# Performance work log

Hardware: AMD Instinct MI355X
Metric: run time of the kernel (lower is better)

The kernel has to match this reference:

```python
import jax, jax.numpy as jnp
import numpy as np

HIDDEN = 128

def setup_inputs() -> dict:
    key = jax.random.key(0)
    ks = jax.random.split(key, 7)
    B, T, I, O = 256, 512, 256, 1000
    s_ih = 1.0 / np.sqrt(HIDDEN)
    x = jax.random.normal(ks[0], (B, T, I), dtype=jnp.float32)
    W_ih = jax.random.uniform(ks[1], (HIDDEN, I), minval=-s_ih, maxval=s_ih, dtype=jnp.float32)
    W_hh = jax.random.uniform(ks[2], (HIDDEN, HIDDEN), minval=-s_ih, maxval=s_ih, dtype=jnp.float32)
    b_ih = jax.random.uniform(ks[3], (HIDDEN,), minval=-s_ih, maxval=s_ih, dtype=jnp.float32)
    b_hh = jax.random.uniform(ks[4], (HIDDEN,), minval=-s_ih, maxval=s_ih, dtype=jnp.float32)
    s_fc = 1.0 / np.sqrt(HIDDEN)
    W_fc = jax.random.uniform(ks[5], (O, HIDDEN), minval=-s_fc, maxval=s_fc, dtype=jnp.float32)
    b_fc = jax.random.uniform(ks[6], (O,), minval=-s_fc, maxval=s_fc, dtype=jnp.float32)
    return {"x": x, "W_ih": W_ih, "W_hh": W_hh, "b_ih": b_ih, "b_hh": b_hh, "W_fc": W_fc, "b_fc": b_fc}


def reference(x, W_ih, W_hh, b_ih, b_hh, W_fc, b_fc):
    B = x.shape[0]
    # Precompute input projection for all timesteps in one big GEMM: [B,T,H]
    xp = jnp.einsum('bti,hi->bth', x, W_ih) + b_ih + b_hh
    h0 = jnp.zeros((B, HIDDEN), dtype=x.dtype)

    def step(h, xp_t):
        h = jnp.tanh(xp_t + h @ W_hh.T)
        return h, None

    # scan over time axis; only the final hidden state feeds the fc head
    h_last, _ = jax.lax.scan(step, h0, jnp.swapaxes(xp, 0, 1))
    return h_last @ W_fc.T + b_fc
```

## Files before the change

### kernel.cpp

```cpp
#include <hip/hip_runtime.h>


#define HID    128
#define TSTEPS 512
#define BATCH  256
#define INDIM  256
#define ODIM   1000

typedef __attribute__((ext_vector_type(8))) short bf16x8;
typedef __attribute__((ext_vector_type(4))) float f32x4;

__device__ __forceinline__ unsigned fb(float f) { return __float_as_uint(f); }
__device__ __forceinline__ float    bf(unsigned u) { return __uint_as_float(u); }
__device__ __forceinline__ unsigned hipair(unsigned e0, unsigned e1) {
    return __builtin_amdgcn_perm(e1, e0, 0x07060302u);
}
__device__ __forceinline__ unsigned rne(unsigned u) {
    return u + 0x7FFFu + ((u >> 16) & 1u);
}
__device__ __forceinline__ float tanh_fast(float p) {
    float v = fminf(fmaxf(p, -15.f), 15.f);
    float e = __expf(2.f * v);
    return 1.f - 2.f * __builtin_amdgcn_rcpf(e + 1.f);
}

__global__ __launch_bounds__(256) void k_phase1(const float* __restrict__ x,
                                                const float* __restrict__ Wih,
                                                const float* __restrict__ bih,
                                                const float* __restrict__ bhh,
                                                float* __restrict__ xp) {
    __shared__ __align__(16) unsigned short xs[2][4096];
    __shared__ __align__(16) unsigned short whs[2][4096];
    __shared__ __align__(16) unsigned short wls[2][4096];

    const int tid  = threadIdx.x;
    const int wave = tid >> 6, lane = tid & 63;
    const int quad = lane >> 4, l16 = lane & 15;
    const int wm = wave >> 1, wn = wave & 1;
    const int m0 = blockIdx.x * 128;

    int srow[4], scol[4], sdst[4];
#pragma unroll
    for (int q = 0; q < 4; q++) {
        int li = q * 256 + tid;
        srow[q] = li >> 3;
        scol[q] = li & 7;
        sdst[q] = srow[q] * 32 + ((((scol[q] >> 1) ^ srow[q]) & 3) << 3) + ((scol[q] & 1) << 2);
    }

    float bias_v[4];
#pragma unroll
    for (int nt = 0; nt < 4; nt++) {
        int j = wn * 64 + nt * 16 + l16;
        bias_v[nt] = bih[j] + bhh[j];
    }

    float4 rx[4], rw[4];
#define LOAD_STAGE(KC)                                                              \
    {                                                                               \
        _Pragma("unroll") for (int q = 0; q < 4; q++) {                             \
            rx[q] = *(const float4*)(x + (size_t)(m0 + srow[q]) * INDIM + (KC) * 32 + scol[q] * 4); \
            rw[q] = *(const float4*)(Wih + (size_t)srow[q] * INDIM + (KC) * 32 + scol[q] * 4);      \
        }                                                                           \
    }
#define WRITE_STAGE(BUF)                                                            \
    {                                                                               \
        _Pragma("unroll") for (int q = 0; q < 4; q++) {                             \
            uint2 px;                                                               \
            px.x = hipair(rne(fb(rx[q].x)), rne(fb(rx[q].y)));                      \
            px.y = hipair(rne(fb(rx[q].z)), rne(fb(rx[q].w)));                      \
            *(uint2*)&xs[BUF][sdst[q]] = px;                                        \
            unsigned u0 = fb(rw[q].x) & 0xFFFF0000u, u1 = fb(rw[q].y) & 0xFFFF0000u;\
            unsigned u2 = fb(rw[q].z) & 0xFFFF0000u, u3 = fb(rw[q].w) & 0xFFFF0000u;\
            unsigned v0 = fb(rw[q].x - bf(u0)), v1 = fb(rw[q].y - bf(u1));          \
            unsigned v2 = fb(rw[q].z - bf(u2)), v3 = fb(rw[q].w - bf(u3));          \
            uint2 ph, pl;                                                           \
            ph.x = hipair(u0, u1); ph.y = hipair(u2, u3);                           \
            pl.x = hipair(v0, v1); pl.y = hipair(v2, v3);                           \
            *(uint2*)&whs[BUF][sdst[q]] = ph;                                       \
            *(uint2*)&wls[BUF][sdst[q]] = pl;                                       \
        }                                                                           \
    }

    f32x4 acc[4][4];
#pragma unroll
    for (int mt = 0; mt < 4; mt++)
#pragma unroll
        for (int nt = 0; nt < 4; nt++) {
            acc[mt][nt].x = 0.f; acc[mt][nt].y = 0.f;
            acc[mt][nt].z = 0.f; acc[mt][nt].w = 0.f;
        }

    LOAD_STAGE(0);
    WRITE_STAGE(0);
    __syncthreads();

    for (int kc = 0; kc < 8; kc++) {
        const int b = kc & 1;
        if (kc < 7) LOAD_STAGE(kc + 1);

        bf16x8 a[4], bh[4], bl[4];
#pragma unroll
        for (int mt = 0; mt < 4; mt++) {
            int row = wm * 64 + mt * 16 + l16;
            a[mt] = *(const bf16x8*)&xs[b][row * 32 + (((quad ^ row) & 3) << 3)];
        }
#pragma unroll
        for (int nt = 0; nt < 4; nt++) {
            int row = wn * 64 + nt * 16 + l16;
            int ad  = row * 32 + (((quad ^ row) & 3) << 3);
            bh[nt] = *(const bf16x8*)&whs[b][ad];
            bl[nt] = *(const bf16x8*)&wls[b][ad];
        }
#pragma unroll
        for (int mt = 0; mt < 4; mt++)
#pragma unroll
            for (int nt = 0; nt < 4; nt++) {
                acc[mt][nt] = __builtin_amdgcn_mfma_f32_16x16x32_bf16(a[mt], bh[nt], acc[mt][nt], 0, 0, 0);
                acc[mt][nt] = __builtin_amdgcn_mfma_f32_16x16x32_bf16(a[mt], bl[nt], acc[mt][nt], 0, 0, 0);
            }

        if (kc < 7) WRITE_STAGE(b ^ 1);
        __syncthreads();
    }

#pragma unroll
    for (int mt = 0; mt < 4; mt++)
#pragma unroll
        for (int nt = 0; nt < 4; nt++)
#pragma unroll
            for (int reg = 0; reg < 4; reg++) {
                int row = m0 + wm * 64 + mt * 16 + quad * 4 + reg;
                xp[(size_t)row * HID + wn * 64 + nt * 16 + l16] = acc[mt][nt][reg] + bias_v[nt];
            }
#undef LOAD_STAGE
#undef WRITE_STAGE
}

#define RNN_STEP3(TV, XQI, XQC, PB) {                                             \
    _Pragma("unroll") for (int reg = 0; reg < 4; reg++) {                         \
        float hv = tanh_fast(C[reg]);                                             \
        unsigned u = rne(fb(hv));                                                 \
        int m = quad * 4 + reg;                                                   \
        hp[PB][m * 128 + ((((jbase >> 3) ^ m) & 15) << 3) + (jbase & 7)] =        \
            (unsigned short)(u >> 16);                                            \
    }                                                                             \
    if ((TV) + 4 < TSTEPS) {                                                      \
        _Pragma("unroll") for (int reg = 0; reg < 4; reg++)                       \
            XQI[reg] = xpb[ib[reg] + ((TV) + 4) * HID];                           \
    }                                                                             \
    __syncthreads();                                                              \
    bf16x8 A[4];                                                                  \
    _Pragma("unroll") for (int kc = 0; kc < 4; kc++)                              \
        A[kc] = *(const bf16x8*)&hp[PB][l16 * 128 + ((((kc * 4 + quad) ^ l16) & 15) << 3)]; \
    f32x4 ch, cl;                                                                 \
    ch.x = XQC[0]; ch.y = XQC[1]; ch.z = XQC[2]; ch.w = XQC[3];                   \
    cl.x = 0.f; cl.y = 0.f; cl.z = 0.f; cl.w = 0.f;                               \
    _Pragma("unroll") for (int kc = 0; kc < 4; kc++) {                            \
        ch = __builtin_amdgcn_mfma_f32_16x16x32_bf16(A[kc], Bh[kc], ch, 0, 0, 0); \
        cl = __builtin_amdgcn_mfma_f32_16x16x32_bf16(A[kc], Bl[kc], cl, 0, 0, 0); \
    }                                                                             \
    C = ch + cl;                                                                  \
}

__global__ __launch_bounds__(512) void k_rnn3(const float* __restrict__ Whh,
                                              float* __restrict__ ws) {
    __shared__ __align__(16) unsigned short hp[2][16 * 128];
    const int tid  = threadIdx.x;
    const int wave = tid >> 6, lane = tid & 63;
    const int quad = lane >> 4, l16 = lane & 15;
    const int r0    = blockIdx.x * 16;
    const int jbase = wave * 16 + l16;

    bf16x8 Bh[4], Bl[4];
#pragma unroll
    for (int kc = 0; kc < 4; kc++) {
        const float* p = Whh + (size_t)jbase * HID + kc * 32 + quad * 8;
        float e[8];
        *(float4*)&e[0] = *(const float4*)p;
        *(float4*)&e[4] = *(const float4*)(p + 4);
        unsigned hu[8], lu[8];
#pragma unroll
        for (int i = 0; i < 8; i++) {
            unsigned u = fb(e[i]), hm = u & 0xFFFF0000u;
            hu[i] = hm;
            lu[i] = fb(e[i] - bf(hm));
        }
        union { unsigned u[4]; bf16x8 v; } th, tl;
#pragma unroll
        for (int q = 0; q < 4; q++) {
            th.u[q] = hipair(hu[2 * q], hu[2 * q + 1]);
            tl.u[q] = hipair(lu[2 * q], lu[2 * q + 1]);
        }
        Bh[kc] = th.v; Bl[kc] = tl.v;
    }

    const float* xpb = ws;
    int ib[4];
#pragma unroll
    for (int reg = 0; reg < 4; reg++)
        ib[reg] = (r0 + quad * 4 + reg) * (TSTEPS * HID) + jbase;

    f32x4 C;
    float xq0[4], xq1[4], xq2[4], xq3[4];
    C.x = xpb[ib[0]]; C.y = xpb[ib[1]]; C.z = xpb[ib[2]]; C.w = xpb[ib[3]];
#pragma unroll
    for (int reg = 0; reg < 4; reg++) {
        xq1[reg] = xpb[ib[reg] + 1 * HID];
        xq2[reg] = xpb[ib[reg] + 2 * HID];
        xq3[reg] = xpb[ib[reg] + 3 * HID];
    }

    for (int t = 0; t < 508; t += 4) {
        RNN_STEP3(t,     xq0, xq1, 0);
        RNN_STEP3(t + 1, xq1, xq2, 1);
        RNN_STEP3(t + 2, xq2, xq3, 0);
        RNN_STEP3(t + 3, xq3, xq0, 1);
    }
    RNN_STEP3(508, xq0, xq1, 0);
    RNN_STEP3(509, xq1, xq2, 1);
    RNN_STEP3(510, xq2, xq3, 0);

#pragma unroll
    for (int reg = 0; reg < 4; reg++)
        ws[ib[reg]] = tanh_fast(C[reg]);
}

__global__ __launch_bounds__(256) void k_fc(const float* __restrict__ ws,
                                            const float* __restrict__ Wfc,
                                            const float* __restrict__ bfc,
                                            float* __restrict__ out) {
    __shared__ float hb[HID];
    const int b   = blockIdx.x;
    const int tid = threadIdx.x;
    if (tid < HID) hb[tid] = ws[(size_t)b * (TSTEPS * HID) + tid];
    __syncthreads();

    for (int o = tid; o < ODIM; o += 256) {
        const float* wr = Wfc + (size_t)o * HID;
        float acc = 0.f;
#pragma unroll
        for (int q = 0; q < 32; q++) {
            float4 wv = *(const float4*)(wr + q * 4);
            float4 hv = *(const float4*)&hb[q * 4];
            acc += wv.x * hv.x + wv.y * hv.y + wv.z * hv.z + wv.w * hv.w;
        }
        out[(size_t)b * ODIM + o] = acc + bfc[o];
    }
}

extern "C" void kernel_launch(void* const* d_in, const int* in_sizes, int n_in,
                              void* d_out, int out_size, void* d_ws, size_t ws_size,
                              hipStream_t stream) {
    const float* x   = (const float*)d_in[0];
    const float* Wih = (const float*)d_in[1];
    const float* Whh = (const float*)d_in[2];
    const float* bih = (const float*)d_in[3];
    const float* bhh = (const float*)d_in[4];
    const float* Wfc = (const float*)d_in[5];
    const float* bfc = (const float*)d_in[6];
    float* out = (float*)d_out;
    float* ws  = (float*)d_ws;

    k_phase1<<<dim3(1024), dim3(256), 0, stream>>>(x, Wih, bih, bhh, ws);
    k_rnn3  <<<dim3(16),   dim3(512), 0, stream>>>(Whh, ws);
    k_fc    <<<dim3(BATCH), dim3(256), 0, stream>>>(ws, Wfc, bfc, out);
}
```

Baseline: 424.3 us.

## Switch GEMM and recurrence MFMAs from split bf16 to single fp16

Replaces the bf16 hi/lo weight split (two MFMAs per tile) with a single fp16 operand in both the input-projection GEMM and the recurrent step, halving MFMA count and LDS traffic for weights. The recurrence step now runs four MFMAs in two independent accumulator chains instead of eight. tanh clamping is removed and conversion uses packed round-toward-zero fp16. This risks accuracy drift from fp16 range and precision in the weights, activations and the 512-step recurrence.

```diff
diff --git a/kernel.cpp b/kernel.cpp
--- a/kernel.cpp
+++ b/kernel.cpp
@@ -7,21 +7,19 @@
 #define INDIM  256
 #define ODIM   1000
 
-typedef __attribute__((ext_vector_type(8))) short bf16x8;
-typedef __attribute__((ext_vector_type(4))) float f32x4;
-
-__device__ __forceinline__ unsigned fb(float f) { return __float_as_uint(f); }
-__device__ __forceinline__ float    bf(unsigned u) { return __uint_as_float(u); }
-__device__ __forceinline__ unsigned hipair(unsigned e0, unsigned e1) {
-    return __builtin_amdgcn_perm(e1, e0, 0x07060302u);
-}
-__device__ __forceinline__ unsigned rne(unsigned u) {
-    return u + 0x7FFFu + ((u >> 16) & 1u);
-}
-__device__ __forceinline__ float tanh_fast(float p) {
-    float v = fminf(fmaxf(p, -15.f), 15.f);
+typedef _Float16 f16x8 __attribute__((ext_vector_type(8)));
+typedef __fp16   fp16x2 __attribute__((ext_vector_type(2)));
+typedef float    f32x4 __attribute__((ext_vector_type(4)));
+
+__device__ __forceinline__ unsigned pk16(float a, float b) {
+    union { fp16x2 h; unsigned u; } t;
+    t.h = __builtin_amdgcn_cvt_pkrtz(a, b);
+    return t.u;
+}
+__device__ __forceinline__ float tanh_fast(float v) {
     float e = __expf(2.f * v);
-    return 1.f - 2.f * __builtin_amdgcn_rcpf(e + 1.f);
+    float r = __builtin_amdgcn_rcpf(e + 1.f);
+    return __builtin_fmaf(-2.f, r, 1.f);
 }
 
 __global__ __launch_bounds__(256) void k_phase1(const float* __restrict__ x,
@@ -29,9 +27,8 @@
                                                 const float* __restrict__ bih,
                                                 const float* __restrict__ bhh,
                                                 float* __restrict__ xp) {
-    __shared__ __align__(16) unsigned short xs[2][4096];
-    __shared__ __align__(16) unsigned short whs[2][4096];
-    __shared__ __align__(16) unsigned short wls[2][4096];
+    __shared__ __align__(16) _Float16 xs[2][4096];
+    __shared__ __align__(16) _Float16 wsm[2][4096];
 
     const int tid  = threadIdx.x;
     const int wave = tid >> 6, lane = tid & 63;
@@ -66,19 +63,11 @@
 #define WRITE_STAGE(BUF)                                                            \
     {                                                                               \
         _Pragma("unroll") for (int q = 0; q < 4; q++) {                             \
-            uint2 px;                                                               \
-            px.x = hipair(rne(fb(rx[q].x)), rne(fb(rx[q].y)));                      \
-            px.y = hipair(rne(fb(rx[q].z)), rne(fb(rx[q].w)));                      \
-            *(uint2*)&xs[BUF][sdst[q]] = px;                                        \
-            unsigned u0 = fb(rw[q].x) & 0xFFFF0000u, u1 = fb(rw[q].y) & 0xFFFF0000u;\
-            unsigned u2 = fb(rw[q].z) & 0xFFFF0000u, u3 = fb(rw[q].w) & 0xFFFF0000u;\
-            unsigned v0 = fb(rw[q].x - bf(u0)), v1 = fb(rw[q].y - bf(u1));          \
-            unsigned v2 = fb(rw[q].z - bf(u2)), v3 = fb(rw[q].w - bf(u3));          \
-            uint2 ph, pl;                                                           \
-            ph.x = hipair(u0, u1); ph.y = hipair(u2, u3);                           \
-            pl.x = hipair(v0, v1); pl.y = hipair(v2, v3);                           \
-            *(uint2*)&whs[BUF][sdst[q]] = ph;                                       \
-            *(uint2*)&wls[BUF][sdst[q]] = pl;                                       \
+            uint2 px, pw;                                                           \
+            px.x = pk16(rx[q].x, rx[q].y); px.y = pk16(rx[q].z, rx[q].w);           \
+            pw.x = pk16(rw[q].x, rw[q].y); pw.y = pk16(rw[q].z, rw[q].w);           \
+            *(uint2*)&xs[BUF][sdst[q]]  = px;                                       \
+            *(uint2*)&wsm[BUF][sdst[q]] = pw;                                       \
         }                                                                           \
     }
 
@@ -99,26 +88,22 @@
         const int b = kc & 1;
         if (kc < 7) LOAD_STAGE(kc + 1);
 
-        bf16x8 a[4], bh[4], bl[4];
+        f16x8 a[4], bw[4];
 #pragma unroll
         for (int mt = 0; mt < 4; mt++) {
             int row = wm * 64 + mt * 16 + l16;
-            a[mt] = *(const bf16x8*)&xs[b][row * 32 + (((quad ^ row) & 3) << 3)];
+            a[mt] = *(const f16x8*)&xs[b][row * 32 + (((quad ^ row) & 3) << 3)];
         }
 #pragma unroll
         for (int nt = 0; nt < 4; nt++) {
             int row = wn * 64 + nt * 16 + l16;
-            int ad  = row * 32 + (((quad ^ row) & 3) << 3);
-            bh[nt] = *(const bf16x8*)&whs[b][ad];
-            bl[nt] = *(const bf16x8*)&wls[b][ad];
+            bw[nt] = *(const f16x8*)&wsm[b][row * 32 + (((quad ^ row) & 3) << 3)];
         }
 #pragma unroll
         for (int mt = 0; mt < 4; mt++)
 #pragma unroll
-            for (int nt = 0; nt < 4; nt++) {
-                acc[mt][nt] = __builtin_amdgcn_mfma_f32_16x16x32_bf16(a[mt], bh[nt], acc[mt][nt], 0, 0, 0);
-                acc[mt][nt] = __builtin_amdgcn_mfma_f32_16x16x32_bf16(a[mt], bl[nt], acc[mt][nt], 0, 0, 0);
-            }
+            for (int nt = 0; nt < 4; nt++)
+                acc[mt][nt] = __builtin_amdgcn_mfma_f32_16x16x32_f16(a[mt], bw[nt], acc[mt][nt], 0, 0, 0);
 
         if (kc < 7) WRITE_STAGE(b ^ 1);
         __syncthreads();
@@ -137,62 +122,49 @@
 #undef WRITE_STAGE
 }
 
-#define RNN_STEP3(TV, XQI, XQC, PB) {                                             \
+#define RNN_STEP4(TV, XQI, XQC, PB) {                                             \
     _Pragma("unroll") for (int reg = 0; reg < 4; reg++) {                         \
         float hv = tanh_fast(C[reg]);                                             \
-        unsigned u = rne(fb(hv));                                                 \
         int m = quad * 4 + reg;                                                   \
         hp[PB][m * 128 + ((((jbase >> 3) ^ m) & 15) << 3) + (jbase & 7)] =        \
-            (unsigned short)(u >> 16);                                            \
+            (_Float16)hv;                                                         \
     }                                                                             \
     if ((TV) + 4 < TSTEPS) {                                                      \
         _Pragma("unroll") for (int reg = 0; reg < 4; reg++)                       \
             XQI[reg] = xpb[ib[reg] + ((TV) + 4) * HID];                           \
     }                                                                             \
     __syncthreads();                                                              \
-    bf16x8 A[4];                                                                  \
+    f16x8 A[4];                                                                   \
     _Pragma("unroll") for (int kc = 0; kc < 4; kc++)                              \
-        A[kc] = *(const bf16x8*)&hp[PB][l16 * 128 + ((((kc * 4 + quad) ^ l16) & 15) << 3)]; \
+        A[kc] = *(const f16x8*)&hp[PB][l16 * 128 + ((((kc * 4 + quad) ^ l16) & 15) << 3)]; \
     f32x4 ch, cl;                                                                 \
     ch.x = XQC[0]; ch.y = XQC[1]; ch.z = XQC[2]; ch.w = XQC[3];                   \
     cl.x = 0.f; cl.y = 0.f; cl.z = 0.f; cl.w = 0.f;                               \
-    _Pragma("unroll") for (int kc = 0; kc < 4; kc++) {                            \
-        ch = __builtin_amdgcn_mfma_f32_16x16x32_bf16(A[kc], Bh[kc], ch, 0, 0, 0); \
-        cl = __builtin_amdgcn_mfma_f32_16x16x32_bf16(A[kc], Bl[kc], cl, 0, 0, 0); \
-    }                                                                             \
+    ch = __builtin_amdgcn_mfma_f32_16x16x32_f16(A[0], Bf[0], ch, 0, 0, 0);        \
+    cl = __builtin_amdgcn_mfma_f32_16x16x32_f16(A[2], Bf[2], cl, 0, 0, 0);        \
+    ch = __builtin_amdgcn_mfma_f32_16x16x32_f16(A[1], Bf[1], ch, 0, 0, 0);        \
+    cl = __builtin_amdgcn_mfma_f32_16x16x32_f16(A[3], Bf[3], cl, 0, 0, 0);        \
     C = ch + cl;                                                                  \
 }
 
-__global__ __launch_bounds__(512) void k_rnn3(const float* __restrict__ Whh,
+__global__ __launch_bounds__(512) void k_rnn4(const float* __restrict__ Whh,
                                               float* __restrict__ ws) {
-    __shared__ __align__(16) unsigned short hp[2][16 * 128];
+    __shared__ __align__(16) _Float16 hp[2][16 * 128];
     const int tid  = threadIdx.x;
     const int wave = tid >> 6, lane = tid & 63;
     const int quad = lane >> 4, l16 = lane & 15;
     const int r0    = blockIdx.x * 16;
     const int jbase = wave * 16 + l16;
 
-    bf16x8 Bh[4], Bl[4];
+    f16x8 Bf[4];
 #pragma unroll
     for (int kc = 0; kc < 4; kc++) {
         const float* p = Whh + (size_t)jbase * HID + kc * 32 + quad * 8;
-        float e[8];
-        *(float4*)&e[0] = *(const float4*)p;
-        *(float4*)&e[4] = *(const float4*)(p + 4);
-        unsigned hu[8], lu[8];
-#pragma unroll
-        for (int i = 0; i < 8; i++) {
-            unsigned u = fb(e[i]), hm = u & 0xFFFF0000u;
-            hu[i] = hm;
-            lu[i] = fb(e[i] - bf(hm));
-        }
-        union { unsigned u[4]; bf16x8 v; } th, tl;
-#pragma unroll
-        for (int q = 0; q < 4; q++) {
-            th.u[q] = hipair(hu[2 * q], hu[2 * q + 1]);
-            tl.u[q] = hipair(lu[2 * q], lu[2 * q + 1]);
-        }
-        Bh[kc] = th.v; Bl[kc] = tl.v;
+        float4 e0 = *(const float4*)p, e1 = *(const float4*)(p + 4);
+        union { unsigned u[4]; f16x8 v; } t;
+        t.u[0] = pk16(e0.x, e0.y); t.u[1] = pk16(e0.z, e0.w);
+        t.u[2] = pk16(e1.x, e1.y); t.u[3] = pk16(e1.z, e1.w);
+        Bf[kc] = t.v;
     }
 
     const float* xpb = ws;
@@ -212,14 +184,14 @@
     }
 
     for (int t = 0; t < 508; t += 4) {
-        RNN_STEP3(t,     xq0, xq1, 0);
-        RNN_STEP3(t + 1, xq1, xq2, 1);
-        RNN_STEP3(t + 2, xq2, xq3, 0);
-        RNN_STEP3(t + 3, xq3, xq0, 1);
-    }
-    RNN_STEP3(508, xq0, xq1, 0);
-    RNN_STEP3(509, xq1, xq2, 1);
-    RNN_STEP3(510, xq2, xq3, 0);
+        RNN_STEP4(t,     xq0, xq1, 0);
+        RNN_STEP4(t + 1, xq1, xq2, 1);
+        RNN_STEP4(t + 2, xq2, xq3, 0);
+        RNN_STEP4(t + 3, xq3, xq0, 1);
+    }
+    RNN_STEP4(508, xq0, xq1, 0);
+    RNN_STEP4(509, xq1, xq2, 1);
+    RNN_STEP4(510, xq2, xq3, 0);
 
 #pragma unroll
     for (int reg = 0; reg < 4; reg++)
@@ -263,6 +235,6 @@
     float* ws  = (float*)d_ws;
 
     k_phase1<<<dim3(1024), dim3(256), 0, stream>>>(x, Wih, bih, bhh, ws);
-    k_rnn3  <<<dim3(16),   dim3(512), 0, stream>>>(Whh, ws);
+    k_rnn4  <<<dim3(16),   dim3(512), 0, stream>>>(Whh, ws);
     k_fc    <<<dim3(BATCH), dim3(256), 0, stream>>>(ws, Wfc, bfc, out);
 }
```

New measurement: 393.0 us. 1.08x faster.
